# Performance work log

Measured on AMD Instinct MI355X. Metric: run time of the kernel, lower is better.

Reference implementation:

```python
import jax, jax.numpy as jnp
import numpy as np

N = 50000
E = 800000
F_IN = 10
H = 256          # hidden
NH = 8           # num heads
HD = H // NH     # head dim
ED = 3           # edge feat dim
L = 3            # num layers
EPS_LN = 1e-5


def setup_inputs() -> dict:
    key = jax.random.key(0)
    ks = jax.random.split(key, 20)
    def g(k, shape, scale=0.05):
        return jax.random.normal(k, shape, dtype=jnp.float32) * scale
    inp = {
        "x": jax.random.normal(ks[0], (N, F_IN), dtype=jnp.float32),
        "edge_attr": jax.random.normal(ks[1], (E, ED), dtype=jnp.float32),
        # input projection
        "W_in": g(ks[2], (F_IN, H)), "b_in": jnp.zeros((H,), jnp.float32),
        # per-layer conv params stacked on leading L axis
        "Wq": g(ks[3], (L, H, H)), "Wk": g(ks[4], (L, H, H)), "Wv": g(ks[5], (L, H, H)),
        "We": g(ks[6], (L, ED, NH)),
        "Wo": g(ks[7], (L, H, H)), "bo": jnp.zeros((L, H), jnp.float32),
        "Wm": g(ks[8], (L, 2 * H, H)), "bm": jnp.zeros((L, H), jnp.float32),
        "gamma": jnp.ones((L, H), jnp.float32), "beta": jnp.zeros((L, H), jnp.float32),
        # output head
        "W_h1": g(ks[9], (H, H // 2)), "b_h1": jnp.zeros((H // 2,), jnp.float32),
        "W_h2": g(ks[10], (H // 2, 1)), "b_h2": jnp.zeros((1,), jnp.float32),
        "edge_index": jax.random.randint(ks[11], (2, E), 0, N, dtype=jnp.int64),
    }
    return inp


def _layer_norm(h, gamma, beta):
    mu = jnp.mean(h, axis=-1, keepdims=True)
    var = jnp.var(h, axis=-1, keepdims=True)
    return (h - mu) * jax.lax.rsqrt(var + EPS_LN) * gamma + beta


def _forward(x, edge_attr, W_in, b_in, Wq, Wk, Wv, We, Wo, bo, Wm, bm,
             gamma, beta, W_h1, b_h1, W_h2, b_h2, src, dst):
    scale = HD ** (-0.5)
    h = jax.nn.relu(x @ W_in + b_in)                       # (N, H)
    for l in range(L):
        Q = (h @ Wq[l]).reshape(N, NH, HD)
        K = (h @ Wk[l]).reshape(N, NH, HD)
        V = (h @ Wv[l]).reshape(N, NH, HD)
        edge_bias = edge_attr @ We[l]                      # (E, NH)
        attn = jnp.sum(Q[dst] * K[src], axis=-1) * scale + edge_bias
        attn = jax.nn.leaky_relu(attn, negative_slope=0.2)
        # global-max stabilization, exactly as the torch code does
        attn_exp = jnp.exp(attn - jnp.max(attn))           # (E, NH)
        attn_sum = jax.ops.segment_sum(attn_exp, dst, num_segments=N)
        attn_norm = attn_exp / jnp.clip(attn_sum[dst], 1e-12, None)
        weighted_V = V[src] * attn_norm[..., None]         # (E, NH, HD)
        agg = jax.ops.segment_sum(weighted_V, dst, num_segments=N)
        agg = agg.reshape(N, H) @ Wo[l] + bo[l]
        upd = jax.nn.relu(jnp.concatenate([h, agg], axis=1) @ Wm[l] + bm[l])
        h = _layer_norm(h + upd, gamma[l], beta[l])
    return jax.nn.relu(h @ W_h1 + b_h1) @ W_h2 + b_h2      # (N, 1) logits


def reference(x, edge_attr, W_in, b_in, Wq, Wk, Wv, We, Wo, bo, Wm, bm,
              gamma, beta, W_h1, b_h1, W_h2, b_h2, edge_index):
    src = edge_index[0]
    dst = edge_index[1]
    return _forward(x, edge_attr, W_in, b_in, Wq, Wk, Wv, We, Wo, bo, Wm, bm,
                    gamma, beta, W_h1, b_h1, W_h2, b_h2, src, dst)
```

## Files before the change

kernel.cpp:

```cpp
#include <hip/hip_runtime.h>
#include <math.h>

#define N_NODES 50000
#define E_EDGES 800000
#define HDIM 256
#define NHEADS 8
#define HEADD 32
#define EDGED 3
#define NLAYERS 3

typedef unsigned int u32;
typedef unsigned char u8;
typedef unsigned short ushort_t;
typedef __attribute__((ext_vector_type(8))) short short8;
typedef __attribute__((ext_vector_type(8))) unsigned short ushort8v;
typedef __attribute__((ext_vector_type(4))) float float4v;
typedef __attribute__((ext_vector_type(2))) float float2v;

typedef __attribute__((address_space(1))) const void* gas_p;
typedef __attribute__((address_space(3))) void* las_p;

__device__ __forceinline__ float bf2f(ushort_t u) {
  union { u32 i; float f; } v;
  v.i = ((u32)u) << 16;
  return v.f;
}
__device__ __forceinline__ ushort_t f2bf(float f) {
  u32 u = __float_as_uint(f);
  u = (u + 0x7FFF + ((u >> 16) & 1)) >> 16;
  return (ushort_t)u;
}
__device__ __forceinline__ u8 f2f8(float f) {
  int p = __builtin_amdgcn_cvt_pk_fp8_f32(f, 0.f, 0, false);
  return (u8)(p & 0xFF);
}
__device__ __forceinline__ void f8x4_to_f32(u32 v, float* out) {
  float2v a = __builtin_amdgcn_cvt_pk_f32_fp8((int)v, false);
  float2v b = __builtin_amdgcn_cvt_pk_f32_fp8((int)v, true);
  out[0] = a[0];
  out[1] = a[1];
  out[2] = b[0];
  out[3] = b[1];
}

__global__ __launch_bounds__(256) void detect_idx_k(const u32* __restrict__ w,
                                                    int* __restrict__ flag) {
  __shared__ u32 sm[256];
  u32 mx = 0;
  for (int k = threadIdx.x; k < 4096; k += 256) mx = max(mx, w[2 * k + 1]);
  sm[threadIdx.x] = mx;
  __syncthreads();
  for (int s = 128; s > 0; s >>= 1) {
    if (threadIdx.x < s)
      sm[threadIdx.x] = max(sm[threadIdx.x], sm[threadIdx.x + s]);
    __syncthreads();
  }
  if (threadIdx.x == 0) flag[0] = (sm[0] == 0) ? 1 : 0;
}

__global__ __launch_bounds__(256) void convert_hist_k(
    const u32* __restrict__ w, const int* __restrict__ flag,
    int* __restrict__ src32, int* __restrict__ dst32, int* __restrict__ dcnt,
    int E_) {
  int e = blockIdx.x * blockDim.x + threadIdx.x;
  if (e >= E_) return;
  int s, d;
  if (flag[0]) {
    s = (int)w[2 * e];
    d = (int)w[2 * (E_ + e)];
  } else {
    s = (int)w[e];
    d = (int)w[E_ + e];
  }
  src32[e] = s;
  dst32[e] = d;
  atomicAdd(&dcnt[d], 1);
}

__global__ __launch_bounds__(256) void scan1_k(const int* __restrict__ deg,
                                               int* __restrict__ scanned,
                                               int* __restrict__ bsum, int n) {
  __shared__ int tmp[256];
  int tid = threadIdx.x;
  int i = blockIdx.x * 256 + tid;
  tmp[tid] = (i < n) ? deg[i] : 0;
  __syncthreads();
  for (int off = 1; off < 256; off <<= 1) {
    int t = (tid >= off) ? tmp[tid - off] : 0;
    __syncthreads();
    tmp[tid] += t;
    __syncthreads();
  }
  if (i < n) scanned[i] = tmp[tid];
  if (tid == 255) bsum[blockIdx.x] = tmp[255];
}

__global__ __launch_bounds__(256) void scan2_k(int* __restrict__ bsum, int nb) {
  __shared__ int tmp[256];
  int tid = threadIdx.x;
  tmp[tid] = (tid < nb) ? bsum[tid] : 0;
  __syncthreads();
  for (int off = 1; off < 256; off <<= 1) {
    int t = (tid >= off) ? tmp[tid - off] : 0;
    __syncthreads();
    tmp[tid] += t;
    __syncthreads();
  }
  if (tid < nb) bsum[tid] = tmp[tid];
}

__global__ __launch_bounds__(256) void scan3_k(const int* __restrict__ scanned,
                                               const int* __restrict__ bsum,
                                               int* __restrict__ rowptr, int n) {
  int i = blockIdx.x * 256 + threadIdx.x;
  if (i < n)
    rowptr[i + 1] = scanned[i] + (blockIdx.x > 0 ? bsum[blockIdx.x - 1] : 0);
  if (i == 0) rowptr[0] = 0;
}

__global__ __launch_bounds__(256) void fill_k(
    const int* __restrict__ srcI, const int* __restrict__ dstI,
    const int* __restrict__ rowptr, int* __restrict__ cursor,
    int2* __restrict__ erec, int E_) {
  int e = blockIdx.x * blockDim.x + threadIdx.x;
  if (e >= E_) return;
  int d = dstI[e];
  int p = rowptr[d] + atomicAdd(&cursor[d], 1);
  erec[p] = make_int2(srcI[e], e);
}

__global__ __launch_bounds__(256) void wprep_all_k(
    const float* __restrict__ Wq, const float* __restrict__ Wk,
    const float* __restrict__ Wv, const float* __restrict__ Wm,
    const float* __restrict__ Wh1, const float* __restrict__ Wo,
    const float* __restrict__ bo, const float* __restrict__ bm,
    ushort_t* __restrict__ WqkvT, ushort_t* __restrict__ WmT,
    ushort_t* __restrict__ Wh1T, float* __restrict__ bcomb) {
  int z = blockIdx.z;
  if (z < 13) {
    const float* W;
    ushort_t* WT;
    int K, N;
    if (z < 9) {
      if (blockIdx.x >= 16) return;
      int l = z / 3, mm = z % 3;
      W = (mm == 0 ? Wq : mm == 1 ? Wk : Wv) + (size_t)l * 65536;
      WT = WqkvT + ((size_t)l * 3 + mm) * 65536;
      K = 256;
      N = 256;
    } else if (z < 12) {
      if (blockIdx.x >= 16) return;
      int l = z - 9;
      W = Wm + (size_t)l * 131072;
      WT = WmT + (size_t)l * 131072;
      K = 512;
      N = 256;
    } else {
      if (blockIdx.x >= 16 || blockIdx.y >= 2) return;
      W = Wh1;
      WT = Wh1T;
      K = 256;
      N = 128;
    }
    __shared__ float t[64][17];
    int k0 = blockIdx.x * 16, n0 = blockIdx.y * 64;
    int tid = threadIdx.x;
    int r = tid >> 6, c = tid & 63;
#pragma unroll
    for (int i = 0; i < 4; ++i)
      t[c][r + 4 * i] = W[(size_t)(k0 + r + 4 * i) * N + n0 + c];
    __syncthreads();
    int nn = tid >> 2, j4 = (tid & 3) * 4;
    ushort4 o;
    o.x = f2bf(t[nn][j4 + 0]);
    o.y = f2bf(t[nn][j4 + 1]);
    o.z = f2bf(t[nn][j4 + 2]);
    o.w = f2bf(t[nn][j4 + 3]);
    *(ushort4*)&WT[(size_t)(n0 + nn) * K + k0 + j4] = o;
  } else if (z < 16) {
    if (blockIdx.x >= 4 || blockIdx.y >= 4) return;
    int l = z - 13;
    const float* A = Wo + (size_t)l * 65536;
    const float* B = Wm + (size_t)l * 131072 + 65536;
    ushort_t* Out = WmT + (size_t)l * 131072;
    __shared__ float As[16][64];
    __shared__ float Bs[16][64];
    int tid = threadIdx.x;
    int tx = tid & 15, ty = tid >> 4;
    int k0 = blockIdx.x * 64, n0 = blockIdx.y * 64;
    float acc[4][4] = {};
    int arow = tid >> 2;
    int aj = (tid & 3) * 4;
    int brow = tid >> 4;
    int bcol = (tid & 15) * 4;
    for (int j0 = 0; j0 < 256; j0 += 16) {
      float4 av = *(const float4*)(A + (size_t)(k0 + arow) * 256 + j0 + aj);
      As[aj + 0][arow] = av.x;
      As[aj + 1][arow] = av.y;
      As[aj + 2][arow] = av.z;
      As[aj + 3][arow] = av.w;
      *(float4*)&Bs[brow][bcol] =
          *(const float4*)(B + (size_t)(j0 + brow) * 256 + n0 + bcol);
      __syncthreads();
#pragma unroll
      for (int j = 0; j < 16; ++j) {
        float a[4], bb[4];
#pragma unroll
        for (int i = 0; i < 4; ++i) a[i] = As[j][ty * 4 + i];
#pragma unroll
        for (int jj = 0; jj < 4; ++jj) bb[jj] = Bs[j][tx * 4 + jj];
#pragma unroll
        for (int i = 0; i < 4; ++i)
#pragma unroll
          for (int jj = 0; jj < 4; ++jj) acc[i][jj] += a[i] * bb[jj];
      }
      __syncthreads();
    }
#pragma unroll
    for (int i = 0; i < 4; ++i)
#pragma unroll
      for (int jj = 0; jj < 4; ++jj) {
        int k = k0 + ty * 4 + i, nn = n0 + tx * 4 + jj;
        Out[(size_t)nn * 512 + 256 + k] = f2bf(acc[i][jj]);
      }
  } else {
    if (blockIdx.x >= 3 || blockIdx.y != 0) return;
    int l = blockIdx.x;
    int nn = threadIdx.x;
    const float* Bw = Wm + (size_t)l * 131072 + 65536;
    const float* bol = bo + l * 256;
    float acc = bm[l * 256 + nn];
    for (int j = 0; j < 256; ++j) acc += bol[j] * Bw[(size_t)j * 256 + nn];
    bcomb[l * 256 + nn] = acc;
  }
}

__global__ __launch_bounds__(256) void input_proj_k(
    const float* __restrict__ x, const float* __restrict__ W,
    const float* __restrict__ b, ushort_t* __restrict__ hbf, int n) {
  __shared__ float ws[10 * 256];
  __shared__ float bs[256];
  int tid = threadIdx.x;
  for (int i = tid; i < 2560; i += 256) ws[i] = W[i];
  bs[tid] = b[tid];
  __syncthreads();
  int row0 = blockIdx.x * 32;
  for (int rr = 0; rr < 32; ++rr) {
    int row = row0 + rr;
    if (row >= n) break;
    float acc = bs[tid];
#pragma unroll
    for (int i = 0; i < 10; ++i) acc += x[row * 10 + i] * ws[i * 256 + tid];
    hbf[(size_t)row * 256 + tid] = f2bf(fmaxf(acc, 0.f));
  }
}

__global__ __launch_bounds__(256) void gemm_qkv_k(
    const ushort_t* __restrict__ A1, const ushort_t* __restrict__ BT,
    ushort_t* __restrict__ Qbf, u8* __restrict__ KV8, int M) {
  const int K1 = 256, Ktot = 256;
  __shared__ __align__(16) ushort_t Als[128 * 64];
  __shared__ __align__(16) ushort_t Bls[128 * 64];
  int tid = threadIdx.x;
  int lane = tid & 63, w = tid >> 6;
  int quad = lane >> 4, m = lane & 15;
  int row0 = blockIdx.y * 128, col0 = blockIdx.x * 128;
  float4v acc[2][8];
#pragma unroll
  for (int t = 0; t < 2; ++t)
#pragma unroll
    for (int j = 0; j < 8; ++j) acc[t][j] = (float4v){0.f, 0.f, 0.f, 0.f};

  int srow = tid >> 3;
  int skc = (tid & 7) * 8;
  char* alsb = (char*)Als + w * 1024;
  char* blsb = (char*)Bls + w * 1024;

  for (int k0 = 0; k0 < Ktot; k0 += 64) {
#pragma unroll
    for (int q = 0; q < 4; ++q) {
      int r = row0 + q * 32 + srow;
      if (r < M) {
        const ushort_t* g = A1 + (size_t)r * K1 + k0 + skc;
        __builtin_amdgcn_global_load_lds((gas_p)g, (las_p)(alsb + q * 4096),
                                         16, 0, 0);
      }
    }
#pragma unroll
    for (int q = 0; q < 4; ++q) {
      const ushort_t* g = BT + (size_t)(col0 + q * 32 + srow) * Ktot + k0 + skc;
      __builtin_amdgcn_global_load_lds((gas_p)g, (las_p)(blsb + q * 4096), 16,
                                       0, 0);
    }
    __syncthreads();
#pragma unroll
    for (int ks = 0; ks < 64; ks += 32) {
      short8 a0 = *(const short8*)&Als[(w * 32 + m) * 64 + ks + quad * 8];
      short8 a1 = *(const short8*)&Als[(w * 32 + 16 + m) * 64 + ks + quad * 8];
#pragma unroll
      for (int j = 0; j < 8; ++j) {
        short8 bj = *(const short8*)&Bls[(16 * j + m) * 64 + ks + quad * 8];
        acc[0][j] =
            __builtin_amdgcn_mfma_f32_16x16x32_bf16(a0, bj, acc[0][j], 0, 0, 0);
        acc[1][j] =
            __builtin_amdgcn_mfma_f32_16x16x32_bf16(a1, bj, acc[1][j], 0, 0, 0);
      }
    }
    __syncthreads();
  }

#pragma unroll
  for (int t = 0; t < 2; ++t) {
#pragma unroll
    for (int j = 0; j < 8; ++j) {
      int col = col0 + 16 * j + m;
#pragma unroll
      for (int rr = 0; rr < 4; ++rr) {
        int row = row0 + w * 32 + 16 * t + quad * 4 + rr;
        if (row >= M) continue;
        float v = acc[t][j][rr];
        if (col < 256)
          Qbf[(size_t)row * 256 + col] = f2bf(v);
        else
          KV8[(size_t)row * 512 + (col - 256)] = f2f8(v);
      }
    }
  }
}

__global__ __launch_bounds__(256) void gemm_ln_k(
    ushort_t* __restrict__ hbf, const ushort_t* __restrict__ aggbf,
    const ushort_t* __restrict__ BT, const float* __restrict__ bcomb,
    const float* __restrict__ gamma, const float* __restrict__ beta, int M) {
  __shared__ __align__(16) ushort_t Als[64 * 64];
  __shared__ __align__(16) ushort_t Bls[256 * 64];
  int tid = threadIdx.x;
  int lane = tid & 63, w = tid >> 6;
  int quad = lane >> 4, m = lane & 15;
  int row0 = blockIdx.x * 64;
  float4v acc[16];
#pragma unroll
  for (int j = 0; j < 16; ++j) acc[j] = (float4v){0.f, 0.f, 0.f, 0.f};

  int srow = tid >> 3;
  int skc = (tid & 7) * 8;
  char* alsb = (char*)Als + w * 1024;
  char* blsb = (char*)Bls + w * 1024;

  for (int k0 = 0; k0 < 512; k0 += 64) {
    const ushort_t* Ap = (k0 < 256) ? (const ushort_t*)hbf : aggbf;
    int kk = k0 & 255;
#pragma unroll
    for (int q = 0; q < 2; ++q) {
      int r = row0 + q * 32 + srow;
      if (r < M) {
        const ushort_t* g = Ap + (size_t)r * 256 + kk + skc;
        __builtin_amdgcn_global_load_lds((gas_p)g, (las_p)(alsb + q * 4096),
                                         16, 0, 0);
      }
    }
#pragma unroll
    for (int q = 0; q < 8; ++q) {
      const ushort_t* g = BT + (size_t)(q * 32 + srow) * 512 + k0 + skc;
      __builtin_amdgcn_global_load_lds((gas_p)g, (las_p)(blsb + q * 4096), 16,
                                       0, 0);
    }
    __syncthreads();
#pragma unroll
    for (int ks = 0; ks < 64; ks += 32) {
      short8 a = *(const short8*)&Als[(w * 16 + m) * 64 + ks + quad * 8];
#pragma unroll
      for (int j = 0; j < 16; ++j) {
        short8 bj = *(const short8*)&Bls[(16 * j + m) * 64 + ks + quad * 8];
        acc[j] = __builtin_amdgcn_mfma_f32_16x16x32_bf16(a, bj, acc[j], 0, 0, 0);
      }
    }
    __syncthreads();
  }

#pragma unroll
  for (int rr = 0; rr < 4; ++rr) {
    int row = row0 + w * 16 + quad * 4 + rr;
    if (row >= M) continue;
    float sv[16];
    float sum = 0.f, sq = 0.f;
#pragma unroll
    for (int j = 0; j < 16; ++j) {
      int col = m + 16 * j;
      float u = fmaxf(acc[j][rr] + bcomb[col], 0.f);
      float s = bf2f(hbf[(size_t)row * 256 + col]) + u;
      sv[j] = s;
      sum += s;
      sq += s * s;
    }
#pragma unroll
    for (int off = 1; off < 16; off <<= 1) {
      sum += __shfl_xor(sum, off);
      sq += __shfl_xor(sq, off);
    }
    float mean = sum * (1.f / 256.f);
    float var = sq * (1.f / 256.f) - mean * mean;
    float r = rsqrtf(var + 1e-5f);
#pragma unroll
    for (int j = 0; j < 16; ++j) {
      int col = m + 16 * j;
      float o = (sv[j] - mean) * r * gamma[col] + beta[col];
      hbf[(size_t)row * 256 + col] = f2bf(o);
    }
  }
}

__global__ __launch_bounds__(256) void head_fused_k(
    const ushort_t* __restrict__ hbf, const ushort_t* __restrict__ W1T,
    const float* __restrict__ b1, const float* __restrict__ W2,
    const float* __restrict__ b2, float* __restrict__ out, int M) {
  __shared__ __align__(16) ushort_t Als[64 * 64];
  __shared__ __align__(16) ushort_t Bls[128 * 64];
  int tid = threadIdx.x;
  int lane = tid & 63, w = tid >> 6;
  int quad = lane >> 4, m = lane & 15;
  int row0 = blockIdx.x * 64;
  float4v acc[8];
#pragma unroll
  for (int j = 0; j < 8; ++j) acc[j] = (float4v){0.f, 0.f, 0.f, 0.f};

  int srow = tid >> 3;
  int skc = (tid & 7) * 8;
  char* alsb = (char*)Als + w * 1024;
  char* blsb = (char*)Bls + w * 1024;

  for (int k0 = 0; k0 < 256; k0 += 64) {
#pragma unroll
    for (int q = 0; q < 2; ++q) {
      int r = row0 + q * 32 + srow;
      if (r < M) {
        const ushort_t* g = hbf + (size_t)r * 256 + k0 + skc;
        __builtin_amdgcn_global_load_lds((gas_p)g, (las_p)(alsb + q * 4096),
                                         16, 0, 0);
      }
    }
#pragma unroll
    for (int q = 0; q < 4; ++q) {
      const ushort_t* g = W1T + (size_t)(q * 32 + srow) * 256 + k0 + skc;
      __builtin_amdgcn_global_load_lds((gas_p)g, (las_p)(blsb + q * 4096), 16,
                                       0, 0);
    }
    __syncthreads();
#pragma unroll
    for (int ks = 0; ks < 64; ks += 32) {
      short8 a = *(const short8*)&Als[(w * 16 + m) * 64 + ks + quad * 8];
#pragma unroll
      for (int j = 0; j < 8; ++j) {
        short8 bj = *(const short8*)&Bls[(16 * j + m) * 64 + ks + quad * 8];
        acc[j] = __builtin_amdgcn_mfma_f32_16x16x32_bf16(a, bj, acc[j], 0, 0, 0);
      }
    }
    __syncthreads();
  }

#pragma unroll
  for (int rr = 0; rr < 4; ++rr) {
    int row = row0 + w * 16 + quad * 4 + rr;
    if (row >= M) continue;
    float p = 0.f;
#pragma unroll
    for (int j = 0; j < 8; ++j) {
      int col = m + 16 * j;
      float t = fmaxf(acc[j][rr] + b1[col], 0.f);
      p += t * W2[col];
    }
#pragma unroll
    for (int off = 1; off < 16; off <<= 1) p += __shfl_xor(p, off);
    if (m == 0) out[row] = p + b2[0];
  }
}

__global__ __launch_bounds__(256) void node_fused_k(
    const ushort_t* __restrict__ Q, const u8* __restrict__ KV8,
    const float* __restrict__ ea, const float* __restrict__ We_l,
    const int* __restrict__ rowptr, const int2* __restrict__ erec,
    ushort_t* __restrict__ agg, int n) {
  int node = (blockIdx.x * blockDim.x + threadIdx.x) >> 6;
  if (node >= n) return;
  int lane = threadIdx.x & 63;
  int hl = lane & 31;
  int slot = lane >> 5;
  ushort8v qu = *((const ushort8v*)(Q + (size_t)node * 256) + hl);
  float q[8];
#pragma unroll
  for (int i = 0; i < 8; ++i) q[i] = bf2f(qu[i]);
  int start = rowptr[node], end = rowptr[node + 1];
  int hh = hl >> 2;
  float w0 = We_l[0 * 8 + hh], w1 = We_l[1 * 8 + hh], w2 = We_l[2 * 8 + hh];
  float l = 0.f;
  float acc[8];
#pragma unroll
  for (int i = 0; i < 8; ++i) acc[i] = 0.f;

  if (end > start) {
    int bp = start + slot;
    int nb = (end - start + 3) >> 2;
    for (int j = 0; j < nb; ++j) {
      int pX = bp + 4 * j;
      int pY = pX + 2;
      bool vX = pX < end, vY = pY < end;
      int2 erX = erec[vX ? pX : start];
      int2 erY = erec[vY ? pY : start];
      const u8* bX = KV8 + (size_t)erX.x * 512;
      const u8* bY = KV8 + (size_t)erY.x * 512;
      uint2 kuX = *((const uint2*)bX + hl);
      uint2 vuX = *((const uint2*)(bX + 256) + hl);
      uint2 kuY = *((const uint2*)bY + hl);
      uint2 vuY = *((const uint2*)(bY + 256) + hl);
      const float* eaX = ea + (size_t)erX.y * 3;
      const float* eaY = ea + (size_t)erY.y * 3;
      float e0X = eaX[0], e1X = eaX[1], e2X = eaX[2];
      float e0Y = eaY[0], e1Y = eaY[1], e2Y = eaY[2];
      float kf[8], vf[8];
      f8x4_to_f32(kuX.x, kf);
      f8x4_to_f32(kuX.y, kf + 4);
      float d = 0.f;
#pragma unroll
      for (int i = 0; i < 8; ++i) d += q[i] * kf[i];
      d += __shfl_xor(d, 1);
      d += __shfl_xor(d, 2);
      float bias = e0X * w0 + e1X * w1 + e2X * w2;
      float a = d * 0.17677669529663687f + bias;
      a = (a > 0.f) ? a : 0.2f * a;
      float wv = vX ? __expf(a) : 0.f;
      f8x4_to_f32(vuX.x, vf);
      f8x4_to_f32(vuX.y, vf + 4);
      l += wv;
#pragma unroll
      for (int i = 0; i < 8; ++i) acc[i] += vf[i] * wv;
      f8x4_to_f32(kuY.x, kf);
      f8x4_to_f32(kuY.y, kf + 4);
      d = 0.f;
#pragma unroll
      for (int i = 0; i < 8; ++i) d += q[i] * kf[i];
      d += __shfl_xor(d, 1);
      d += __shfl_xor(d, 2);
      bias = e0Y * w0 + e1Y * w1 + e2Y * w2;
      a = d * 0.17677669529663687f + bias;
      a = (a > 0.f) ? a : 0.2f * a;
      wv = vY ? __expf(a) : 0.f;
      f8x4_to_f32(vuY.x, vf);
      f8x4_to_f32(vuY.y, vf + 4);
      l += wv;
#pragma unroll
      for (int i = 0; i < 8; ++i) acc[i] += vf[i] * wv;
    }
  }
  l += __shfl_xor(l, 32);
  float inv = 1.f / fmaxf(l, 1e-12f);
  ushort8v o;
#pragma unroll
  for (int i = 0; i < 8; ++i) {
    float v = (acc[i] + __shfl_xor(acc[i], 32)) * inv;
    o[i] = f2bf(v);
  }
  if (slot == 0)
    *((ushort8v*)(agg + (size_t)node * 256) + hl) = o;
}

extern "C" void kernel_launch(void* const* d_in, const int* in_sizes, int n_in,
                              void* d_out, int out_size, void* d_ws,
                              size_t ws_size, hipStream_t stream) {
  const float* x = (const float*)d_in[0];
  const float* edge_attr = (const float*)d_in[1];
  const float* W_in = (const float*)d_in[2];
  const float* b_in = (const float*)d_in[3];
  const float* Wq = (const float*)d_in[4];
  const float* Wk = (const float*)d_in[5];
  const float* Wv = (const float*)d_in[6];
  const float* We = (const float*)d_in[7];
  const float* Wo = (const float*)d_in[8];
  const float* bo = (const float*)d_in[9];
  const float* Wm = (const float*)d_in[10];
  const float* bm = (const float*)d_in[11];
  const float* gamma = (const float*)d_in[12];
  const float* beta = (const float*)d_in[13];
  const float* W_h1 = (const float*)d_in[14];
  const float* b_h1 = (const float*)d_in[15];
  const float* W_h2 = (const float*)d_in[16];
  const float* b_h2 = (const float*)d_in[17];
  const u32* eidx_w = (const u32*)d_in[18];

  float* ws = (float*)d_ws;
  const size_t NH_ = (size_t)N_NODES * HDIM;
  ushort_t* hbf = (ushort_t*)ws;
  ushort_t* Qbf = hbf + NH_;
  u8* KV8 = (u8*)(Qbf + NH_);
  ushort_t* aggbf = (ushort_t*)(KV8 + (size_t)N_NODES * 512);
  int* idxflag = (int*)(aggbf + NH_);
  int2* erec = (int2*)(idxflag + 2);
  int* rowptr = (int*)(erec + E_EDGES);
  int* dcnt = rowptr + N_NODES + 1;
  int* cursor = dcnt + N_NODES;
  int* scanned = cursor + N_NODES;
  int* bsum = scanned + N_NODES;
  float* bcomb = (float*)(bsum + 256);
  ushort_t* WT = (ushort_t*)(bcomb + 3 * 256);
  const size_t W64K = (size_t)HDIM * HDIM;
  const size_t W128K = (size_t)2 * HDIM * HDIM;
  ushort_t* WqkvT = WT;
  ushort_t* WmT = WqkvT + 3 * 3 * W64K;
  ushort_t* Wh1T = WmT + 3 * W128K;
  int* srcI = (int*)Qbf;
  int* dstI = srcI + E_EDGES;

  detect_idx_k<<<1, 256, 0, stream>>>(eidx_w, idxflag);
  hipMemsetAsync(dcnt, 0, (size_t)2 * N_NODES * sizeof(int), stream);
  convert_hist_k<<<(E_EDGES + 255) / 256, 256, 0, stream>>>(
      eidx_w, idxflag, srcI, dstI, dcnt, E_EDGES);
  const int nsb = (N_NODES + 255) / 256;
  scan1_k<<<nsb, 256, 0, stream>>>(dcnt, scanned, bsum, N_NODES);
  scan2_k<<<1, 256, 0, stream>>>(bsum, nsb);
  scan3_k<<<nsb, 256, 0, stream>>>(scanned, bsum, rowptr, N_NODES);
  fill_k<<<(E_EDGES + 255) / 256, 256, 0, stream>>>(
      srcI, dstI, rowptr, cursor, erec, E_EDGES);

  wprep_all_k<<<dim3(16, 4, 17), 256, 0, stream>>>(
      Wq, Wk, Wv, Wm, W_h1, Wo, bo, bm, WqkvT, WmT, Wh1T, bcomb);

  input_proj_k<<<(N_NODES + 31) / 32, 256, 0, stream>>>(x, W_in, b_in, hbf,
                                                        N_NODES);
  dim3 gqkv(768 / 128, (N_NODES + 127) / 128);
  const int gml = (N_NODES + 63) / 64;
  const int nodewave_grid = (N_NODES * 64 + 255) / 256;

  for (int l = 0; l < NLAYERS; ++l) {
    const float* We_l = We + (size_t)l * EDGED * NHEADS;

    gemm_qkv_k<<<gqkv, 256, 0, stream>>>(
        hbf, WqkvT + (size_t)l * 3 * W64K, Qbf, KV8, N_NODES);
    node_fused_k<<<nodewave_grid, 256, 0, stream>>>(
        Qbf, KV8, edge_attr, We_l, rowptr, erec, aggbf, N_NODES);
    gemm_ln_k<<<gml, 256, 0, stream>>>(
        hbf, aggbf, WmT + (size_t)l * W128K, bcomb + l * 256,
        gamma + (size_t)l * HDIM, beta + (size_t)l * HDIM, N_NODES);
  }
  head_fused_k<<<gml, 256, 0, stream>>>(hbf, Wh1T, b_h1, W_h2, b_h2,
                                        (float*)d_out, N_NODES);
}
```

Baseline: 793.4 us.

## Keep full A row-tile in LDS across three QKV column tiles; simplify edge loop

The QKV GEMM now loads the whole 128x256 A tile into LDS once and loops over three 128-wide column tiles, so each block covers 384 output columns and the grid width drops from 6 to 2. This cuts repeated global reads of the activation rows, at the cost of 64KB of A in LDS, which lowers occupancy and removes parallelism. Separately, the per-node attention loop goes from two unrolled edges per half-wave per iteration to one edge per iteration with a branch. That reduces register use but exposes less memory-level parallelism on the gathers.

```diff
diff --git a/kernel.cpp b/kernel.cpp
--- a/kernel.cpp
+++ b/kernel.cpp
@@ -258,71 +258,83 @@
 __global__ __launch_bounds__(256) void gemm_qkv_k(
     const ushort_t* __restrict__ A1, const ushort_t* __restrict__ BT,
     ushort_t* __restrict__ Qbf, u8* __restrict__ KV8, int M) {
-  const int K1 = 256, Ktot = 256;
-  __shared__ __align__(16) ushort_t Als[128 * 64];
+  __shared__ __align__(16) ushort_t Als[128 * 256];
   __shared__ __align__(16) ushort_t Bls[128 * 64];
   int tid = threadIdx.x;
   int lane = tid & 63, w = tid >> 6;
   int quad = lane >> 4, m = lane & 15;
-  int row0 = blockIdx.y * 128, col0 = blockIdx.x * 128;
-  float4v acc[2][8];
-#pragma unroll
-  for (int t = 0; t < 2; ++t)
-#pragma unroll
-    for (int j = 0; j < 8; ++j) acc[t][j] = (float4v){0.f, 0.f, 0.f, 0.f};
+  int row0 = blockIdx.y * 128;
+  int colbase = blockIdx.x * 384;
+
+  {
+    int arow = tid >> 5;
+    int akc = (tid & 31) * 8;
+    char* alsb = (char*)Als + w * 1024;
+#pragma unroll
+    for (int q = 0; q < 16; ++q) {
+      int r = row0 + q * 8 + arow;
+      if (r < M) {
+        const ushort_t* g = A1 + (size_t)r * 256 + akc;
+        __builtin_amdgcn_global_load_lds((gas_p)g, (las_p)(alsb + q * 4096),
+                                         16, 0, 0);
+      }
+    }
+  }
 
   int srow = tid >> 3;
   int skc = (tid & 7) * 8;
-  char* alsb = (char*)Als + w * 1024;
   char* blsb = (char*)Bls + w * 1024;
 
-  for (int k0 = 0; k0 < Ktot; k0 += 64) {
-#pragma unroll
-    for (int q = 0; q < 4; ++q) {
-      int r = row0 + q * 32 + srow;
-      if (r < M) {
-        const ushort_t* g = A1 + (size_t)r * K1 + k0 + skc;
-        __builtin_amdgcn_global_load_lds((gas_p)g, (las_p)(alsb + q * 4096),
+  for (int cj = 0; cj < 3; ++cj) {
+    int col0 = colbase + cj * 128;
+    float4v acc[2][8];
+#pragma unroll
+    for (int t = 0; t < 2; ++t)
+#pragma unroll
+      for (int j = 0; j < 8; ++j) acc[t][j] = (float4v){0.f, 0.f, 0.f, 0.f};
+
+    for (int k0 = 0; k0 < 256; k0 += 64) {
+#pragma unroll
+      for (int q = 0; q < 4; ++q) {
+        const ushort_t* g =
+            BT + (size_t)(col0 + q * 32 + srow) * 256 + k0 + skc;
+        __builtin_amdgcn_global_load_lds((gas_p)g, (las_p)(blsb + q * 4096),
                                          16, 0, 0);
       }
-    }
-#pragma unroll
-    for (int q = 0; q < 4; ++q) {
-      const ushort_t* g = BT + (size_t)(col0 + q * 32 + srow) * Ktot + k0 + skc;
-      __builtin_amdgcn_global_load_lds((gas_p)g, (las_p)(blsb + q * 4096), 16,
-                                       0, 0);
-    }
-    __syncthreads();
-#pragma unroll
-    for (int ks = 0; ks < 64; ks += 32) {
-      short8 a0 = *(const short8*)&Als[(w * 32 + m) * 64 + ks + quad * 8];
-      short8 a1 = *(const short8*)&Als[(w * 32 + 16 + m) * 64 + ks + quad * 8];
+      __syncthreads();
+#pragma unroll
+      for (int ks = 0; ks < 64; ks += 32) {
+        short8 a0 =
+            *(const short8*)&Als[(w * 32 + m) * 256 + k0 + ks + quad * 8];
+        short8 a1 =
+            *(const short8*)&Als[(w * 32 + 16 + m) * 256 + k0 + ks + quad * 8];
+#pragma unroll
+        for (int j = 0; j < 8; ++j) {
+          short8 bj = *(const short8*)&Bls[(16 * j + m) * 64 + ks + quad * 8];
+          acc[0][j] = __builtin_amdgcn_mfma_f32_16x16x32_bf16(a0, bj,
+                                                              acc[0][j], 0, 0, 0);
+          acc[1][j] = __builtin_amdgcn_mfma_f32_16x16x32_bf16(a1, bj,
+                                                              acc[1][j], 0, 0, 0);
+        }
+      }
+      __syncthreads();
+    }
+
+#pragma unroll
+    for (int t = 0; t < 2; ++t) {
 #pragma unroll
       for (int j = 0; j < 8; ++j) {
-        short8 bj = *(const short8*)&Bls[(16 * j + m) * 64 + ks + quad * 8];
-        acc[0][j] =
-            __builtin_amdgcn_mfma_f32_16x16x32_bf16(a0, bj, acc[0][j], 0, 0, 0);
-        acc[1][j] =
-            __builtin_amdgcn_mfma_f32_16x16x32_bf16(a1, bj, acc[1][j], 0, 0, 0);
-      }
-    }
-    __syncthreads();
-  }
-
-#pragma unroll
-  for (int t = 0; t < 2; ++t) {
-#pragma unroll
-    for (int j = 0; j < 8; ++j) {
-      int col = col0 + 16 * j + m;
-#pragma unroll
-      for (int rr = 0; rr < 4; ++rr) {
-        int row = row0 + w * 32 + 16 * t + quad * 4 + rr;
-        if (row >= M) continue;
-        float v = acc[t][j][rr];
-        if (col < 256)
-          Qbf[(size_t)row * 256 + col] = f2bf(v);
-        else
-          KV8[(size_t)row * 512 + (col - 256)] = f2f8(v);
+        int col = col0 + 16 * j + m;
+#pragma unroll
+        for (int rr = 0; rr < 4; ++rr) {
+          int row = row0 + w * 32 + 16 * t + quad * 4 + rr;
+          if (row >= M) continue;
+          float v = acc[t][j][rr];
+          if (col < 256)
+            Qbf[(size_t)row * 256 + col] = f2bf(v);
+          else
+            KV8[(size_t)row * 512 + (col - 256)] = f2f8(v);
+        }
       }
     }
   }
@@ -497,55 +509,30 @@
 #pragma unroll
   for (int i = 0; i < 8; ++i) acc[i] = 0.f;
 
-  if (end > start) {
-    int bp = start + slot;
-    int nb = (end - start + 3) >> 2;
-    for (int j = 0; j < nb; ++j) {
-      int pX = bp + 4 * j;
-      int pY = pX + 2;
-      bool vX = pX < end, vY = pY < end;
-      int2 erX = erec[vX ? pX : start];
-      int2 erY = erec[vY ? pY : start];
-      const u8* bX = KV8 + (size_t)erX.x * 512;
-      const u8* bY = KV8 + (size_t)erY.x * 512;
-      uint2 kuX = *((const uint2*)bX + hl);
-      uint2 vuX = *((const uint2*)(bX + 256) + hl);
-      uint2 kuY = *((const uint2*)bY + hl);
-      uint2 vuY = *((const uint2*)(bY + 256) + hl);
-      const float* eaX = ea + (size_t)erX.y * 3;
-      const float* eaY = ea + (size_t)erY.y * 3;
-      float e0X = eaX[0], e1X = eaX[1], e2X = eaX[2];
-      float e0Y = eaY[0], e1Y = eaY[1], e2Y = eaY[2];
+  int iters = (end - start + 1) >> 1;
+  for (int it = 0; it < iters; ++it) {
+    int p = start + 2 * it + slot;
+    if (p < end) {
+      int2 er = erec[p];
+      const u8* base = KV8 + (size_t)er.x * 512;
+      uint2 ku = *((const uint2*)base + hl);
+      uint2 vu = *((const uint2*)(base + 256) + hl);
       float kf[8], vf[8];
-      f8x4_to_f32(kuX.x, kf);
-      f8x4_to_f32(kuX.y, kf + 4);
+      f8x4_to_f32(ku.x, kf);
+      f8x4_to_f32(ku.y, kf + 4);
+      f8x4_to_f32(vu.x, vf);
+      f8x4_to_f32(vu.y, vf + 4);
       float d = 0.f;
 #pragma unroll
       for (int i = 0; i < 8; ++i) d += q[i] * kf[i];
       d += __shfl_xor(d, 1);
       d += __shfl_xor(d, 2);
-      float bias = e0X * w0 + e1X * w1 + e2X * w2;
+      float bias = ea[(size_t)er.y * 3 + 0] * w0 +
+                   ea[(size_t)er.y * 3 + 1] * w1 +
+                   ea[(size_t)er.y * 3 + 2] * w2;
       float a = d * 0.17677669529663687f + bias;
       a = (a > 0.f) ? a : 0.2f * a;
-      float wv = vX ? __expf(a) : 0.f;
-      f8x4_to_f32(vuX.x, vf);
-      f8x4_to_f32(vuX.y, vf + 4);
-      l += wv;
-#pragma unroll
-      for (int i = 0; i < 8; ++i) acc[i] += vf[i] * wv;
-      f8x4_to_f32(kuY.x, kf);
-      f8x4_to_f32(kuY.y, kf + 4);
-      d = 0.f;
-#pragma unroll
-      for (int i = 0; i < 8; ++i) d += q[i] * kf[i];
-      d += __shfl_xor(d, 1);
-      d += __shfl_xor(d, 2);
-      bias = e0Y * w0 + e1Y * w1 + e2Y * w2;
-      a = d * 0.17677669529663687f + bias;
-      a = (a > 0.f) ? a : 0.2f * a;
-      wv = vY ? __expf(a) : 0.f;
-      f8x4_to_f32(vuY.x, vf);
-      f8x4_to_f32(vuY.y, vf + 4);
+      float wv = __expf(a);
       l += wv;
 #pragma unroll
       for (int i = 0; i < 8; ++i) acc[i] += vf[i] * wv;
@@ -625,7 +612,7 @@
 
   input_proj_k<<<(N_NODES + 31) / 32, 256, 0, stream>>>(x, W_in, b_in, hbf,
                                                         N_NODES);
-  dim3 gqkv(768 / 128, (N_NODES + 127) / 128);
+  dim3 gqkv(2, (N_NODES + 127) / 128);
   const int gml = (N_NODES + 63) / 64;
   const int nodewave_grid = (N_NODES * 64 + 255) / 256;
 
```

Measured after the change: 830.2 us. +4.6%, slower.
